# Optimization experiments

Hardware: AMD Instinct MI355X
Metric: run time of the kernel (lower is better)

The kernel has to match this reference:

```python
import jax, jax.numpy as jnp
import numpy as np


def setup_inputs() -> dict:
    key = jax.random.key(0)
    kq, kk, kv = jax.random.split(key, 3)
    B, L, Q, H, E = 8, 128, 8, 8, 64
    S, P = 128, 8
    queries = jax.random.normal(kq, (B, L, Q, H, E), dtype=jnp.float32)
    keys = jax.random.normal(kk, (B, S, P, H, E), dtype=jnp.float32)
    values = jax.random.normal(kv, (B, S, P, H, E), dtype=jnp.float32)
    attn_mask = jnp.zeros((1,), dtype=bool)  # unused by the module
    return {"queries": queries, "keys": keys, "values": values, "attn_mask": attn_mask}


def reference(queries, keys, values, attn_mask):
    # queries: [B,L,Q,H,E]; keys/values: [B,S,P,H,E]
    B, L, Q, H, E = queries.shape
    S, P = values.shape[1], values.shape[2]
    scale = 1.0 / np.sqrt(E).astype(np.float32)
    # scores: [B,S,P,L,Q,H]
    scores = jnp.einsum('blqhe,bsphe->bsplqh', queries, keys)
    # softmax over joint (S,P) axis
    scaled = (scale * scores).reshape(B, S * P, L, Q, H)
    attn = jax.nn.softmax(scaled, axis=1).reshape(B, S, P, L, Q, H)
    # dropout is identity in eval / with p=0.0
    V = jnp.einsum('bsphe,bsplqh->blqhe', values, attn)
    return V
```

## Files before the change

kernel.cpp:

```cpp
#include <hip/hip_runtime.h>
#include <hip/hip_bf16.h>

typedef __attribute__((ext_vector_type(4))) float f32x4;
typedef __attribute__((ext_vector_type(16))) float f32x16;
typedef __attribute__((ext_vector_type(8))) short bf16x8;
typedef __attribute__((ext_vector_type(4))) unsigned u32x4;

#define MFMA32(a, b, c) __builtin_amdgcn_mfma_f32_32x32x16_bf16(a, b, c, 0, 0, 0)

constexpr int Bc = 8, Hc = 8;
constexpr int NQ = 1024;
constexpr int NK = 1024;
constexpr int RS = 512;
constexpr int Ec = 64;
constexpr int KT = 128;
constexpr int NT = NK / KT;
constexpr float QSCALE = 0.125f;

__device__ __forceinline__ short f2bf(float x) {
    return (short)__builtin_bit_cast(unsigned short, __float2bfloat16(x));
}

__device__ __forceinline__ bf16x8 pack2(float4 a, float4 b) {
    bf16x8 r;
    r[0] = f2bf(a.x); r[1] = f2bf(a.y); r[2] = f2bf(a.z); r[3] = f2bf(a.w);
    r[4] = f2bf(b.x); r[5] = f2bf(b.y); r[6] = f2bf(b.z); r[7] = f2bf(b.w);
    return r;
}

__device__ __forceinline__ bf16x8 pack2s(float4 a, float4 b, float s) {
    bf16x8 r;
    r[0] = f2bf(a.x * s); r[1] = f2bf(a.y * s); r[2] = f2bf(a.z * s); r[3] = f2bf(a.w * s);
    r[4] = f2bf(b.x * s); r[5] = f2bf(b.y * s); r[6] = f2bf(b.z * s); r[7] = f2bf(b.w * s);
    return r;
}

__device__ __forceinline__ unsigned cvtpk(float a, float b) {
    unsigned lo = (unsigned short)__builtin_bit_cast(unsigned short, __float2bfloat16(a));
    unsigned hi = (unsigned short)__builtin_bit_cast(unsigned short, __float2bfloat16(b));
    return lo | (hi << 16);
}

__device__ __forceinline__ void gload16(const short* src, short* dst) {
    __builtin_amdgcn_global_load_lds((const __attribute__((address_space(1))) void*)src,
                                     (__attribute__((address_space(3))) void*)dst, 16, 0, 0);
}

__global__ __launch_bounds__(256, 4)
void cvt_kv(const float* __restrict__ Kg, const float* __restrict__ Vg,
            short* __restrict__ Kbf, short* __restrict__ Vt) {
    __shared__ __attribute__((aligned(16))) short Vl[64][72];
    const int tid  = threadIdx.x;
    const int head = blockIdx.x >> 4;
    const int kb   = blockIdx.x & 15;
    const int b    = head >> 3, h = head & 7;
    const int row  = tid >> 2, q = tid & 3;

    const size_t gin = (((size_t)(b * NK + kb * 64 + row)) * 8 + h) * 64 + q * 16;
    const float4* kp = (const float4*)(Kg + gin);
    float4 k0 = kp[0], k1 = kp[1], k2 = kp[2], k3 = kp[3];
    short* kout = Kbf + ((size_t)head * NK + kb * 64 + row) * 64 + q * 16;
    ((bf16x8*)kout)[0] = pack2(k0, k1);
    ((bf16x8*)kout)[1] = pack2(k2, k3);

    const float4* vp = (const float4*)(Vg + gin);
    float4 v0 = vp[0], v1 = vp[1], v2 = vp[2], v3 = vp[3];
    const float vv[16] = {v0.x, v0.y, v0.z, v0.w, v1.x, v1.y, v1.z, v1.w,
                          v2.x, v2.y, v2.z, v2.w, v3.x, v3.y, v3.z, v3.w};
#pragma unroll
    for (int j = 0; j < 16; ++j) Vl[q * 16 + j][row] = f2bf(vv[j]);
    __syncthreads();
    short* vout = Vt + ((size_t)head * Ec + row) * NK + kb * 64 + q * 16;
    ((bf16x8*)vout)[0] = *(const bf16x8*)&Vl[row][q * 16];
    ((bf16x8*)vout)[1] = *(const bf16x8*)&Vl[row][q * 16 + 8];
}

__global__ __launch_bounds__(256, 2)
void fully_attn_kernel(const float* __restrict__ Qg, const short* __restrict__ Kbf,
                       const short* __restrict__ Vt, float* __restrict__ Og) {
    __shared__ __attribute__((aligned(16))) short Kl[2][KT][64];
    __shared__ __attribute__((aligned(16))) short Vl[2][64][KT];

    const int tid  = threadIdx.x;
    const int lane = tid & 63;
    const int wv   = tid >> 6;
    const int ql   = lane & 31;
    const int hi   = lane >> 5;
    const int swz  = (lane & 7) << 4;

    const int bid  = blockIdx.x;
    const int head = (bid & 7) * 8 + (bid >> 6);
    const int qb   = (bid >> 3) & 7;
    const int b    = head >> 3, h = head & 7;

    const size_t headQ = (size_t)b * NQ * RS + (size_t)h * Ec;
    const short* KbfH = Kbf + (size_t)head * NK * Ec;
    const short* VtH  = Vt + (size_t)head * Ec * NK;

    const int qrow = qb * 128 + wv * 32 + ql;
    const float* qp = Qg + headQ + (size_t)qrow * RS;
    bf16x8 qf[4];
#pragma unroll
    for (int j = 0; j < 4; ++j) {
        const float4* q4 = (const float4*)(qp + j * 16 + hi * 8);
        qf[j] = pack2s(q4[0], q4[1], QSCALE);
    }

    const int klocal = lane >> 3;
    const int kj     = (lane & 7) ^ (klocal & 7);
    const int vlocal = lane >> 4;

#define STAGE(buf, tt)                                                            \
    {                                                                             \
        _Pragma("unroll")                                                         \
        for (int s = 0; s < 4; ++s)                                               \
            gload16(KbfH + (size_t)((tt) * KT + wv * 32 + s * 8 + klocal) * 64 +  \
                        kj * 8,                                                   \
                    &Kl[buf][wv * 32 + s * 8][0]);                                \
        _Pragma("unroll")                                                         \
        for (int s = 0; s < 4; ++s)                                               \
            gload16(VtH + (size_t)(wv * 16 + s * 4 + vlocal) * NK + (tt) * KT +   \
                        (((lane & 15) ^ ((s * 4 + vlocal) & 7)) * 8),             \
                    &Vl[buf][wv * 16 + s * 4][0]);                                \
    }

    STAGE(0, 0);
    __syncthreads();

    float m_r = -1e30f, l_r = 0.0f;
    f32x16 o0 = (f32x16)(0.0f), o1 = (f32x16)(0.0f);

    int cur = 0;
    for (int t = 0; t < NT; ++t) {
        if (t + 1 < NT) STAGE(cur ^ 1, t + 1);

        f32x16 p[4];
        __builtin_amdgcn_s_setprio(1);
#pragma unroll
        for (int kt = 0; kt < 4; ++kt) {
            const char* kr = (const char*)&Kl[cur][kt * 32 + ql][0];
            f32x16 acc = (f32x16)(0.0f);
#pragma unroll
            for (int j = 0; j < 4; ++j) {
                bf16x8 kf = *(const bf16x8*)(kr + ((j * 32 + hi * 16) ^ swz));
                acc = MFMA32(kf, qf[j], acc);
            }
            p[kt] = acc;
        }
        __builtin_amdgcn_s_setprio(0);

        float pm = -1e30f;
#pragma unroll
        for (int kt = 0; kt < 4; ++kt)
#pragma unroll
            for (int i = 0; i < 16; ++i) pm = fmaxf(pm, p[kt][i]);
        pm = fmaxf(pm, __shfl_xor(pm, 32));
        const float mn = fmaxf(m_r, pm);
        const float alpha = __expf(m_r - mn);
        float rs = 0.0f;
#pragma unroll
        for (int kt = 0; kt < 4; ++kt)
#pragma unroll
            for (int i = 0; i < 16; ++i) {
                float e = __expf(p[kt][i] - mn);
                p[kt][i] = e;
                rs += e;
            }
        rs += __shfl_xor(rs, 32);
        l_r = l_r * alpha + rs;
        m_r = mn;
#pragma unroll
        for (int i = 0; i < 16; ++i) { o0[i] *= alpha; o1[i] *= alpha; }

        __builtin_amdgcn_s_setprio(1);
#pragma unroll
        for (int m = 0; m < 8; ++m) {
            const int kt = m >> 1, r0 = (m & 1) * 8;
            unsigned a0 = cvtpk(p[kt][r0 + 0], p[kt][r0 + 1]);
            unsigned a1 = cvtpk(p[kt][r0 + 2], p[kt][r0 + 3]);
            unsigned b0 = cvtpk(p[kt][r0 + 4], p[kt][r0 + 5]);
            unsigned b1 = cvtpk(p[kt][r0 + 6], p[kt][r0 + 7]);
            asm("v_permlane32_swap_b32 %0, %1" : "+v"(a0), "+v"(b0));
            asm("v_permlane32_swap_b32 %0, %1" : "+v"(a1), "+v"(b1));
            u32x4 w = {a0, a1, b0, b1};
            bf16x8 pf = __builtin_bit_cast(bf16x8, w);
            const int cb = (m * 32 + hi * 16) ^ swz;
            bf16x8 v0 = *(const bf16x8*)((const char*)&Vl[cur][ql][0] + cb);
            bf16x8 v1 = *(const bf16x8*)((const char*)&Vl[cur][32 + ql][0] + cb);
            o0 = MFMA32(v0, pf, o0);
            o1 = MFMA32(v1, pf, o1);
        }
        __builtin_amdgcn_s_setprio(0);

        __syncthreads();
        cur ^= 1;
    }

    const float inv = 1.0f / l_r;
    float* op = Og + headQ + (size_t)qrow * RS;
#pragma unroll
    for (int i = 0; i < 16; ++i) {
        const int e = (i & 3) + 8 * (i >> 2) + 4 * hi;
        op[e]      = o0[i] * inv;
        op[32 + e] = o1[i] * inv;
    }
}

extern "C" void kernel_launch(void* const* d_in, const int* in_sizes, int n_in,
                              void* d_out, int out_size, void* d_ws, size_t ws_size,
                              hipStream_t stream) {
    const float* Qg = (const float*)d_in[0];
    const float* Kg = (const float*)d_in[1];
    const float* Vg = (const float*)d_in[2];
    float* Og = (float*)d_out;

    short* Kbf = (short*)d_ws;
    short* Vt  = (short*)d_ws + (size_t)64 * NK * Ec;

    hipLaunchKernelGGL(cvt_kv, dim3(64 * 16), dim3(256), 0, stream, Kg, Vg, Kbf, Vt);
    hipLaunchKernelGGL(fully_attn_kernel, dim3(512), dim3(256), 0, stream,
                       Qg, Kbf, Vt, Og);
}
```

Baseline: 47.04 us.

## Use exp2 softmax with deferred rescaling, hoist LDS fragment loads, vectorize stores

Folds log2(e) into the query scale so the softmax uses exp2. Online-softmax rescaling of the accumulators is skipped unless the wave's max rises by more than a threshold, and the per-tile row-sum shuffle moves to a single reduction at the end. K and V fragments are loaded from LDS into registers ahead of their MFMA loops, and output writes become float4 stores. This trims VALU and exp work and the cross-lane traffic per tile, but raises register pressure and lets exponents grow up to 2^8 before rescaling.

```diff
diff --git a/kernel.cpp b/kernel.cpp
--- a/kernel.cpp
+++ b/kernel.cpp
@@ -1,5 +1,6 @@
 #include <hip/hip_runtime.h>
 #include <hip/hip_bf16.h>
+#include <math.h>
 
 typedef __attribute__((ext_vector_type(4))) float f32x4;
 typedef __attribute__((ext_vector_type(16))) float f32x16;
@@ -15,7 +16,8 @@
 constexpr int Ec = 64;
 constexpr int KT = 128;
 constexpr int NT = NK / KT;
-constexpr float QSCALE = 0.125f;
+constexpr float QSCALE2 = 0.125f * 1.4426950408889634f;
+constexpr float DEFER_THR = 8.0f;
 
 __device__ __forceinline__ short f2bf(float x) {
     return (short)__builtin_bit_cast(unsigned short, __float2bfloat16(x));
@@ -103,7 +105,7 @@
 #pragma unroll
     for (int j = 0; j < 4; ++j) {
         const float4* q4 = (const float4*)(qp + j * 16 + hi * 8);
-        qf[j] = pack2s(q4[0], q4[1], QSCALE);
+        qf[j] = pack2s(q4[0], q4[1], QSCALE2);
     }
 
     const int klocal = lane >> 3;
@@ -134,43 +136,64 @@
     for (int t = 0; t < NT; ++t) {
         if (t + 1 < NT) STAGE(cur ^ 1, t + 1);
 
+        bf16x8 kf[4][4];
+#pragma unroll
+        for (int kt = 0; kt < 4; ++kt) {
+            const char* kr = (const char*)&Kl[cur][kt * 32 + ql][0];
+#pragma unroll
+            for (int j = 0; j < 4; ++j)
+                kf[kt][j] = *(const bf16x8*)(kr + ((j * 32 + hi * 16) ^ swz));
+        }
         f32x16 p[4];
         __builtin_amdgcn_s_setprio(1);
 #pragma unroll
         for (int kt = 0; kt < 4; ++kt) {
-            const char* kr = (const char*)&Kl[cur][kt * 32 + ql][0];
             f32x16 acc = (f32x16)(0.0f);
 #pragma unroll
-            for (int j = 0; j < 4; ++j) {
-                bf16x8 kf = *(const bf16x8*)(kr + ((j * 32 + hi * 16) ^ swz));
-                acc = MFMA32(kf, qf[j], acc);
+            for (int j = 0; j < 4; ++j) acc = MFMA32(kf[kt][j], qf[j], acc);
+            p[kt] = acc;
+        }
+        __builtin_amdgcn_s_setprio(0);
+
+        bf16x8 vf0[8], vf1[8];
+#pragma unroll
+        for (int m = 0; m < 8; ++m) {
+            const int cb = (m * 32 + hi * 16) ^ swz;
+            vf0[m] = *(const bf16x8*)((const char*)&Vl[cur][ql][0] + cb);
+            vf1[m] = *(const bf16x8*)((const char*)&Vl[cur][32 + ql][0] + cb);
+        }
+
+        float pm = fmaxf(p[0][0], p[0][1]);
+#pragma unroll
+        for (int kt = 0; kt < 4; ++kt)
+#pragma unroll
+            for (int i = (kt == 0 ? 2 : 0); i < 16; i += 2)
+                pm = fmaxf(fmaxf(p[kt][i], p[kt][i + 1]), pm);
+        pm = fmaxf(pm, __shfl_xor(pm, 32));
+
+        if (!__all(pm <= m_r + DEFER_THR)) {
+            const float mn = fmaxf(m_r, pm);
+            const float alpha = exp2f(m_r - mn);
+            l_r *= alpha;
+#pragma unroll
+            for (int i = 0; i < 16; ++i) { o0[i] *= alpha; o1[i] *= alpha; }
+            m_r = mn;
+        }
+
+        float rs0 = 0.f, rs1 = 0.f, rs2 = 0.f, rs3 = 0.f;
+#pragma unroll
+        for (int kt = 0; kt < 4; ++kt)
+#pragma unroll
+            for (int i = 0; i < 16; i += 4) {
+                float e0 = exp2f(p[kt][i + 0] - m_r);
+                float e1 = exp2f(p[kt][i + 1] - m_r);
+                float e2 = exp2f(p[kt][i + 2] - m_r);
+                float e3 = exp2f(p[kt][i + 3] - m_r);
+                p[kt][i + 0] = e0; p[kt][i + 1] = e1;
+                p[kt][i + 2] = e2; p[kt][i + 3] = e3;
+                rs0 += e0; rs1 += e1; rs2 += e2; rs3 += e3;
             }
-            p[kt] = acc;
-        }
-        __builtin_amdgcn_s_setprio(0);
-
-        float pm = -1e30f;
-#pragma unroll
-        for (int kt = 0; kt < 4; ++kt)
-#pragma unroll
-            for (int i = 0; i < 16; ++i) pm = fmaxf(pm, p[kt][i]);
-        pm = fmaxf(pm, __shfl_xor(pm, 32));
-        const float mn = fmaxf(m_r, pm);
-        const float alpha = __expf(m_r - mn);
-        float rs = 0.0f;
-#pragma unroll
-        for (int kt = 0; kt < 4; ++kt)
-#pragma unroll
-            for (int i = 0; i < 16; ++i) {
-                float e = __expf(p[kt][i] - mn);
-                p[kt][i] = e;
-                rs += e;
-            }
-        rs += __shfl_xor(rs, 32);
-        l_r = l_r * alpha + rs;
-        m_r = mn;
-#pragma unroll
-        for (int i = 0; i < 16; ++i) { o0[i] *= alpha; o1[i] *= alpha; }
+        l_r += (rs0 + rs1) + (rs2 + rs3);
 
         __builtin_amdgcn_s_setprio(1);
 #pragma unroll
@@ -184,11 +207,8 @@
             asm("v_permlane32_swap_b32 %0, %1" : "+v"(a1), "+v"(b1));
             u32x4 w = {a0, a1, b0, b1};
             bf16x8 pf = __builtin_bit_cast(bf16x8, w);
-            const int cb = (m * 32 + hi * 16) ^ swz;
-            bf16x8 v0 = *(const bf16x8*)((const char*)&Vl[cur][ql][0] + cb);
-            bf16x8 v1 = *(const bf16x8*)((const char*)&Vl[cur][32 + ql][0] + cb);
-            o0 = MFMA32(v0, pf, o0);
-            o1 = MFMA32(v1, pf, o1);
+            o0 = MFMA32(vf0[m], pf, o0);
+            o1 = MFMA32(vf1[m], pf, o1);
         }
         __builtin_amdgcn_s_setprio(0);
 
@@ -196,13 +216,17 @@
         cur ^= 1;
     }
 
+    l_r += __shfl_xor(l_r, 32);
     const float inv = 1.0f / l_r;
     float* op = Og + headQ + (size_t)qrow * RS;
 #pragma unroll
-    for (int i = 0; i < 16; ++i) {
-        const int e = (i & 3) + 8 * (i >> 2) + 4 * hi;
-        op[e]      = o0[i] * inv;
-        op[32 + e] = o1[i] * inv;
+    for (int bnk = 0; bnk < 4; ++bnk) {
+        float4 s0 = {o0[bnk * 4 + 0] * inv, o0[bnk * 4 + 1] * inv,
+                     o0[bnk * 4 + 2] * inv, o0[bnk * 4 + 3] * inv};
+        float4 s1 = {o1[bnk * 4 + 0] * inv, o1[bnk * 4 + 1] * inv,
+                     o1[bnk * 4 + 2] * inv, o1[bnk * 4 + 3] * inv};
+        *(float4*)(op + bnk * 8 + hi * 4)      = s0;
+        *(float4*)(op + 32 + bnk * 8 + hi * 4) = s1;
     }
 }
 
```

New measurement: 54.21 us. 15.2% more time.
